# Kernel tuning notes

Hardware: AMD Instinct MI355X
Metric: run time of the kernel (lower is better)

Reference implementation:

```python
import jax, jax.numpy as jnp
import numpy as np

N, E, G = 50000, 400000, 500
F_IN, D_H, D_EMB = 92, 256, 128
EPS = 1e-5

def _ln(x, g, b):
    # per-node LayerNorm over feature dim
    mu = jnp.mean(x, axis=-1, keepdims=True)
    var = jnp.mean(jnp.square(x - mu), axis=-1, keepdims=True)
    return (x - mu) * jax.lax.rsqrt(var + EPS) * g + b

def _gcn_conv(x, src, dst, W, b):
    # PyG GCNConv: add self-loops, symmetric normalization
    xw = x @ W                                    # [N, D_out]
    loop = jnp.arange(N, dtype=src.dtype)
    s = jnp.concatenate([src, loop])              # [E+N]
    d = jnp.concatenate([dst, loop])
    deg = jax.ops.segment_sum(jnp.ones_like(d, dtype=xw.dtype), d, num_segments=N)
    dinv = jnp.where(deg > 0, jax.lax.rsqrt(jnp.maximum(deg, 1.0)) * (deg > 0), 0.0)
    norm = dinv[s] * dinv[d]                      # [E+N]
    msg = xw[s] * norm[:, None]                   # gather + scale
    out = jax.ops.segment_sum(msg, d, num_segments=N)  # scatter-add
    return out + b

def setup_inputs() -> dict:
    key = jax.random.key(0)
    ks = jax.random.split(key, 12)
    def lin(k, fan_in, fan_out):
        bound = 1.0 / np.sqrt(fan_in)
        kw, kb = jax.random.split(k)
        W = jax.random.uniform(kw, (fan_in, fan_out), jnp.float32, -bound, bound)
        b = jax.random.uniform(kb, (fan_out,), jnp.float32, -bound, bound)
        return W, b
    x = jax.random.normal(ks[0], (N, F_IN), jnp.float32)
    edge_index = jax.random.randint(ks[1], (2, E), 0, N, jnp.int32)
    batch = jnp.sort(jax.random.randint(ks[2], (N,), 0, G, jnp.int32))
    nfc_W, nfc_b = lin(ks[3], F_IN, D_H)
    gc1_W, gc1_b = lin(ks[4], D_H, D_H)
    gc2_W, gc2_b = lin(ks[5], D_H, D_EMB)
    fc1_W, fc1_b = lin(ks[6], D_EMB, 64)
    fc2_W, fc2_b = lin(ks[7], 64, 1)
    return {
        "x": x, "edge_index": edge_index, "batch": batch,
        "nfc_W": nfc_W, "nfc_b": nfc_b,
        "gn1_g": jnp.ones((D_H,), jnp.float32), "gn1_b": jnp.zeros((D_H,), jnp.float32),
        "gc1_W": gc1_W, "gc1_b": gc1_b,
        "gn2_g": jnp.ones((D_EMB,), jnp.float32), "gn2_b": jnp.zeros((D_EMB,), jnp.float32),
        "gc2_W": gc2_W, "gc2_b": gc2_b,
        "fc1_W": fc1_W, "fc1_b": fc1_b,
        "fc2_W": fc2_W, "fc2_b": fc2_b,
    }

def reference(x, edge_index, batch, nfc_W, nfc_b, gn1_g, gn1_b, gc1_W, gc1_b,
              gn2_g, gn2_b, gc2_W, gc2_b, fc1_W, fc1_b, fc2_W, fc2_b):
    src, dst = edge_index[0], edge_index[1]
    lrelu = jax.nn.leaky_relu  # slope 0.01, matches F.leaky_relu default
    ha = lrelu(x @ nfc_W + nfc_b)
    ha = lrelu(_ln(_gcn_conv(ha, src, dst, gc1_W, gc1_b), gn1_g, gn1_b))
    ha = lrelu(_ln(_gcn_conv(ha, src, dst, gc2_W, gc2_b), gn2_g, gn2_b))
    # F.normalize(p=2, dim=1)
    ha = ha / jnp.maximum(jnp.linalg.norm(ha, axis=1, keepdims=True), 1e-12)
    hg = jax.ops.segment_sum(ha, batch, num_segments=G)   # global_add_pool
    h = lrelu(hg @ fc1_W + fc1_b)
    out = h @ fc2_W + fc2_b
    return out, ha
```

## Files before the change

kernel.cpp:

```cpp
#include <hip/hip_runtime.h>

#define NN 50000
#define EE 400000
#define GG 500
#define F_IN 92
#define KP1 96
#define D_H 256
#define D_EMB 128
#define NB_SCAN 196

typedef __attribute__((ext_vector_type(8))) short short8_t;
typedef __attribute__((ext_vector_type(4))) float floatx4;
typedef unsigned short u16;
typedef unsigned int u32;

__device__ __forceinline__ float lrelu(float v) { return v > 0.f ? v : 0.01f * v; }
__device__ __forceinline__ u16 f2b(float v) {
    union { float f; u32 u; } x; x.f = v;
    u32 r = x.u + 0x7FFFu + ((x.u >> 16) & 1u);
    return (u16)(r >> 16);
}
__device__ __forceinline__ float wave_allsum(float v) {
#pragma unroll
    for (int m = 1; m < 64; m <<= 1) v += __shfl_xor(v, m);
    return v;
}
__device__ __forceinline__ void glds16(const void* g, void* l) {
    __builtin_amdgcn_global_load_lds(
        (const __attribute__((address_space(1))) void*)g,
        (__attribute__((address_space(3))) void*)l, 16, 0, 0);
}

#define WN_ELEMS (D_H * KP1)
#define W1_ELEMS (D_H * D_H)
#define W2_ELEMS (D_EMB * D_H)
#define CAST_BLK ((WN_ELEMS + W1_ELEMS + W2_ELEMS + 255) / 256)
__global__ void cast_count(const float* __restrict__ nfc_W, const float* __restrict__ gc1_W,
                           const float* __restrict__ gc2_W, u16* __restrict__ WtN,
                           u16* __restrict__ Wt1, u16* __restrict__ Wt2,
                           const int* __restrict__ dstE, int* __restrict__ cnt) {
    if ((int)blockIdx.x >= CAST_BLK) {
        int e = (blockIdx.x - CAST_BLK) * 256 + threadIdx.x;
        if (e < EE) atomicAdd(&cnt[dstE[e]], 1);
        return;
    }
    int i = blockIdx.x * blockDim.x + threadIdx.x;
    if (i < WN_ELEMS) {
        int n = i / KP1, k = i % KP1;
        WtN[i] = f2b(k < F_IN ? nfc_W[(long)k * D_H + n] : 0.f);
    } else if (i < WN_ELEMS + W1_ELEMS) {
        int j = i - WN_ELEMS;
        int n = j / D_H, k = j % D_H;
        Wt1[j] = f2b(gc1_W[(long)k * D_H + n]);
    } else if (i < WN_ELEMS + W1_ELEMS + W2_ELEMS) {
        int j = i - WN_ELEMS - W1_ELEMS;
        int n = j / D_H, k = j % D_H;
        Wt2[j] = f2b(gc2_W[(long)k * D_EMB + n]);
    }
}

__global__ __launch_bounds__(256) void gemm_f32a(const float* __restrict__ Af_,
                                                 const u16* __restrict__ Wt,
                                                 const float* __restrict__ bias,
                                                 u16* __restrict__ out,
                                                 const int* __restrict__ cnt,
                                                 int* __restrict__ rowptr,
                                                 int* __restrict__ bsum,
                                                 float* __restrict__ dinv,
                                                 int MBLK) {
    if ((int)blockIdx.x >= MBLK) {
        __shared__ int sm[256];
        int b = blockIdx.x - MBLK;
        int i = b * 256 + threadIdx.x;
        int v = (i < NN) ? cnt[i] : 0;
        if (i < NN) dinv[i] = rsqrtf((float)v + 1.0f);
        sm[threadIdx.x] = v;
        __syncthreads();
#pragma unroll
        for (int off = 1; off < 256; off <<= 1) {
            int t = (threadIdx.x >= off) ? sm[threadIdx.x - off] : 0;
            __syncthreads();
            sm[threadIdx.x] += t;
            __syncthreads();
        }
        if (i < NN) rowptr[i] = sm[threadIdx.x] - v;
        if (threadIdx.x == 255) bsum[b] = sm[255];
        return;
    }
    __shared__ u16 As[64][40];
    __shared__ u16 Bs[256][32];
    int tid = threadIdx.x;
    int wave = tid >> 6, lane = tid & 63;
    int lm = lane & 15, lk = lane >> 4;
    int m0 = blockIdx.x * 64;
    int rowA = tid >> 2, skA = (tid & 3) * 8;
    int lr = lane >> 2, lc = (lane & 3) * 8;
    int gmA = m0 + rowA;
    const float* Af = Af_ + (size_t)gmA * F_IN;
    const u16* Bp[4];
#pragma unroll
    for (int ch = 0; ch < 4; ++ch)
        Bp[ch] = Wt + (size_t)(wave * 64 + ch * 16 + lr) * KP1 + lc;
    floatx4 acc[16] = {};
    for (int k0 = 0; k0 < KP1; k0 += 32) {
        float f[8];
#pragma unroll
        for (int q = 0; q < 2; ++q) {
            int col = k0 + skA + 4 * q;
            float4 t = make_float4(0.f, 0.f, 0.f, 0.f);
            if (gmA < NN && col < F_IN) t = *(const float4*)(Af + col);
            f[4 * q] = t.x; f[4 * q + 1] = t.y; f[4 * q + 2] = t.z; f[4 * q + 3] = t.w;
        }
        u32 pk[4];
#pragma unroll
        for (int t2 = 0; t2 < 4; ++t2)
            pk[t2] = ((u32)f2b(f[2 * t2 + 1]) << 16) | f2b(f[2 * t2]);
        __syncthreads();
        *(uint4*)&As[rowA][skA] = make_uint4(pk[0], pk[1], pk[2], pk[3]);
#pragma unroll
        for (int ch = 0; ch < 4; ++ch)
            glds16(Bp[ch] + k0, &Bs[wave * 64 + ch * 16][0]);
        __syncthreads();
        short8_t af = *(const short8_t*)&As[wave * 16 + lm][lk * 8];
#pragma unroll
        for (int c = 0; c < 16; ++c) {
            short8_t bf = *(const short8_t*)&Bs[c * 16 + lm][lk * 8];
            acc[c] = __builtin_amdgcn_mfma_f32_16x16x32_bf16(af, bf, acc[c], 0, 0, 0);
        }
    }
#pragma unroll
    for (int r = 0; r < 4; ++r) {
        int gm = m0 + wave * 16 + lk * 4 + r;
        if (gm >= NN) continue;
#pragma unroll
        for (int c = 0; c < 16; ++c) {
            int gn = c * 16 + lm;
            float v = acc[c][r] + bias[gn];
            out[(size_t)gm * D_H + gn] = f2b(lrelu(v));
        }
    }
}

__global__ void scan23(int* __restrict__ rowptr, const int* __restrict__ bsum) {
    __shared__ int sm[256];
    int b = blockIdx.x;
    int v = ((int)threadIdx.x < b) ? bsum[threadIdx.x] : 0;
    sm[threadIdx.x] = v;
    __syncthreads();
#pragma unroll
    for (int off = 128; off > 0; off >>= 1) {
        if ((int)threadIdx.x < off) sm[threadIdx.x] += sm[threadIdx.x + off];
        __syncthreads();
    }
    int base = sm[0];
    int i = b * 256 + threadIdx.x;
    if (i < NN) rowptr[i] += base;
    if (i == 0) rowptr[NN] = EE;
}

template <int ND, bool SCAT>
__global__ __launch_bounds__(256) void gemm_glds(const u16* __restrict__ A,
                                                 const u16* __restrict__ Wt,
                                                 const float* __restrict__ rscale,
                                                 u16* __restrict__ out,
                                                 const int* __restrict__ srcE,
                                                 const int* __restrict__ dstE,
                                                 const int* __restrict__ rowptr,
                                                 int* __restrict__ cursor,
                                                 int* __restrict__ esrc,
                                                 int MBLK) {
    if constexpr (SCAT) {
        if ((int)blockIdx.x >= MBLK) {
            int e = (blockIdx.x - MBLK) * 256 + threadIdx.x;
            if (e < EE) {
                int d = dstE[e];
                int p = rowptr[d] + atomicAdd(&cursor[d], 1);
                esrc[p] = srcE[e];
            }
            return;
        }
    }
    constexpr int NC  = ND / 16;
    constexpr int BCH = ND / 64;
    __shared__ u16 As[2][64][32];
    __shared__ u16 Bs[2][ND][32];
    int tid = threadIdx.x;
    int wave = tid >> 6, lane = tid & 63;
    int lm = lane & 15, lk = lane >> 4;
    int m0 = blockIdx.x * 64;
    int lr = lane >> 2;
    int lc = (lane & 3) * 8;
    const int Ka = D_H;
    const u16* Ap = A + (size_t)(m0 + wave * 16 + lr) * Ka + lc;
    const u16* Bp[BCH];
#pragma unroll
    for (int ch = 0; ch < BCH; ++ch)
        Bp[ch] = Wt + (size_t)(wave * (ND / 4) + ch * 16 + lr) * Ka + lc;

    auto stage = [&](int b, int k0) {
        glds16(Ap + k0, &As[b][wave * 16][0]);
#pragma unroll
        for (int ch = 0; ch < BCH; ++ch)
            glds16(Bp[ch] + k0, &Bs[b][wave * (ND / 4) + ch * 16][0]);
    };

    floatx4 acc[NC] = {};
    constexpr int nk = D_H / 32;
    stage(0, 0);
    asm volatile("s_waitcnt vmcnt(0)" ::: "memory");
    __builtin_amdgcn_s_barrier();
    __builtin_amdgcn_sched_barrier(0);
    int cur = 0;
    for (int t = 0; t < nk; ++t) {
        if (t + 1 < nk) stage(cur ^ 1, (t + 1) * 32);
        short8_t af = *(const short8_t*)&As[cur][wave * 16 + lm][lk * 8];
#pragma unroll
        for (int c = 0; c < NC; ++c) {
            short8_t bf = *(const short8_t*)&Bs[cur][c * 16 + lm][lk * 8];
            acc[c] = __builtin_amdgcn_mfma_f32_16x16x32_bf16(af, bf, acc[c], 0, 0, 0);
        }
        if (t + 1 < nk) {
            __builtin_amdgcn_sched_barrier(0);
            asm volatile("s_waitcnt vmcnt(0)" ::: "memory");
            __builtin_amdgcn_s_barrier();
            __builtin_amdgcn_sched_barrier(0);
            cur ^= 1;
        }
    }
#pragma unroll
    for (int r = 0; r < 4; ++r) {
        int gm = m0 + wave * 16 + lk * 4 + r;
        if (gm >= NN) continue;
        float rs = rscale[gm];
#pragma unroll
        for (int c = 0; c < NC; ++c) {
            int gn = c * 16 + lm;
            out[(size_t)gm * ND + gn] = f2b(acc[c][r] * rs);
        }
    }
}

template <int U>
__device__ __forceinline__ void loadrow(const u32* __restrict__ p, u32* r) {
    if constexpr (U == 2) { uint2 t = *(const uint2*)p; r[0] = t.x; r[1] = t.y; }
    else                  { r[0] = *p; }
}
template <int D, bool L2N, bool TOBF, bool POOL>
__global__ __launch_bounds__(256) void agg_ln(const u16* __restrict__ y,
                                              const int* __restrict__ rowptr,
                                              const int* __restrict__ esrc,
                                              const float* __restrict__ dinv,
                                              const float* __restrict__ bias,
                                              const float* __restrict__ gamma,
                                              const float* __restrict__ beta,
                                              u16* __restrict__ outb,
                                              float* __restrict__ outf,
                                              const int* __restrict__ batch,
                                              float* __restrict__ hg) {
    constexpr int V = D / 64;
    constexpr int U = V / 2;
    constexpr int RW = D / 2;
    int wave = threadIdx.x >> 6, lane = threadIdx.x & 63;
    int i = blockIdx.x * 4 + wave;
    if constexpr (!POOL) { if (i >= NN) return; }
    int beg = __builtin_amdgcn_readfirstlane(rowptr[i]);
    int end = __builtin_amdgcn_readfirstlane(rowptr[i + 1]);
    const u32* yu = (const u32*)y;
    const int lu = lane * U;
    float accL[U] = {}, accH[U] = {};
    u32 r[8][U];
    int k = beg;
    for (; k + 7 < end; k += 8) {
#pragma unroll
        for (int q = 0; q < 8; ++q) loadrow<U>(yu + (size_t)esrc[k + q] * RW + lu, r[q]);
#pragma unroll
        for (int j = 0; j < U; ++j) {
            float sL = 0.f, sH = 0.f;
#pragma unroll
            for (int q = 0; q < 8; ++q) {
                sL += __uint_as_float(r[q][j] << 16);
                sH += __uint_as_float(r[q][j] & 0xFFFF0000u);
            }
            accL[j] += sL; accH[j] += sH;
        }
    }
    for (; k + 3 < end; k += 4) {
#pragma unroll
        for (int q = 0; q < 4; ++q) loadrow<U>(yu + (size_t)esrc[k + q] * RW + lu, r[q]);
#pragma unroll
        for (int j = 0; j < U; ++j) {
            accL[j] += (__uint_as_float(r[0][j] << 16) + __uint_as_float(r[1][j] << 16))
                     + (__uint_as_float(r[2][j] << 16) + __uint_as_float(r[3][j] << 16));
            accH[j] += (__uint_as_float(r[0][j] & 0xFFFF0000u) + __uint_as_float(r[1][j] & 0xFFFF0000u))
                     + (__uint_as_float(r[2][j] & 0xFFFF0000u) + __uint_as_float(r[3][j] & 0xFFFF0000u));
        }
    }
    for (; k < end; ++k) {
        loadrow<U>(yu + (size_t)esrc[k] * RW + lu, r[0]);
#pragma unroll
        for (int j = 0; j < U; ++j) {
            accL[j] += __uint_as_float(r[0][j] << 16);
            accH[j] += __uint_as_float(r[0][j] & 0xFFFF0000u);
        }
    }
    loadrow<U>(yu + (size_t)i * RW + lu, r[0]);
#pragma unroll
    for (int j = 0; j < U; ++j) {
        accL[j] += __uint_as_float(r[0][j] << 16);
        accH[j] += __uint_as_float(r[0][j] & 0xFFFF0000u);
    }
    float di = dinv[i];
    float xv[V], lsum = 0.f;
#pragma unroll
    for (int j = 0; j < U; ++j) {
        xv[2 * j]     = accL[j] * di + bias[lane * V + 2 * j];
        xv[2 * j + 1] = accH[j] * di + bias[lane * V + 2 * j + 1];
    }
#pragma unroll
    for (int v = 0; v < V; ++v) lsum += xv[v];
    float mu = wave_allsum(lsum) * (1.0f / D);
    float l2 = 0.f;
#pragma unroll
    for (int v = 0; v < V; ++v) { xv[v] -= mu; l2 += xv[v] * xv[v]; }
    float rstd = rsqrtf(wave_allsum(l2) * (1.0f / D) + 1e-5f);
    float yv[V], ss = 0.f;
#pragma unroll
    for (int v = 0; v < V; ++v) {
        float t = xv[v] * rstd * gamma[lane * V + v] + beta[lane * V + v];
        t = lrelu(t);
        yv[v] = t; ss += t * t;
    }
    if constexpr (L2N) {
        float inv = 1.0f / fmaxf(sqrtf(wave_allsum(ss)), 1e-12f);
#pragma unroll
        for (int v = 0; v < V; ++v) yv[v] *= inv;
    }
    if constexpr (TOBF) {
        if constexpr (V == 4) {
            *(ushort4*)(outb + (size_t)i * D + lane * V) =
                make_ushort4(f2b(yv[0]), f2b(yv[1]), f2b(yv[2]), f2b(yv[3]));
        } else {
            *(ushort2*)(outb + (size_t)i * D + lane * V) = make_ushort2(f2b(yv[0]), f2b(yv[1]));
        }
    } else {
        if constexpr (V == 2) {
            *(float2*)(outf + (size_t)i * D + lane * V) = make_float2(yv[0], yv[1]);
        } else {
            *(float4*)(outf + (size_t)i * D + lane * V) = make_float4(yv[0], yv[1], yv[2], yv[3]);
        }
    }
    if constexpr (POOL) {
        __shared__ float psm[4][D_EMB];
        __shared__ int pb[4];
        psm[wave][lane * 2]     = yv[0];
        psm[wave][lane * 2 + 1] = yv[1];
        if (lane == 0) pb[wave] = batch[i];
        __syncthreads();
        int tid = threadIdx.x;
        if (tid < D_EMB) {
            float acc = psm[0][tid];
            int cur = pb[0];
#pragma unroll
            for (int w = 1; w < 4; ++w) {
                if (pb[w] != cur) {
                    atomicAdd(&hg[(size_t)cur * D_EMB + tid], acc);
                    acc = 0.f; cur = pb[w];
                }
                acc += psm[w][tid];
            }
            atomicAdd(&hg[(size_t)cur * D_EMB + tid], acc);
        }
    }
}

__global__ __launch_bounds__(64) void head_kernel(const float* __restrict__ hg,
                                                  const float* __restrict__ fc1W,
                                                  const float* __restrict__ fc1b,
                                                  const float* __restrict__ fc2W,
                                                  const float* __restrict__ fc2b,
                                                  float* __restrict__ out) {
    int g = blockIdx.x;
    int j = threadIdx.x;
    float h = fc1b[j];
#pragma unroll 8
    for (int k = 0; k < D_EMB; ++k) h += hg[(size_t)g * D_EMB + k] * fc1W[k * 64 + j];
    h = lrelu(h) * fc2W[j];
#pragma unroll
    for (int m = 1; m < 64; m <<= 1) h += __shfl_xor(h, m);
    if (j == 0) out[g] = h + fc2b[0];
}

static inline size_t align256(size_t x) { return (x + 255) & ~(size_t)255; }

extern "C" void kernel_launch(void* const* d_in, const int* in_sizes, int n_in,
                              void* d_out, int out_size, void* d_ws, size_t ws_size,
                              hipStream_t stream) {
    const float* x     = (const float*)d_in[0];
    const int*   ei    = (const int*)d_in[1];
    const int*   batch = (const int*)d_in[2];
    const float* nfc_W = (const float*)d_in[3];
    const float* nfc_b = (const float*)d_in[4];
    const float* gn1_g = (const float*)d_in[5];
    const float* gn1_b = (const float*)d_in[6];
    const float* gc1_W = (const float*)d_in[7];
    const float* gc1_b = (const float*)d_in[8];
    const float* gn2_g = (const float*)d_in[9];
    const float* gn2_b = (const float*)d_in[10];
    const float* gc2_W = (const float*)d_in[11];
    const float* gc2_b = (const float*)d_in[12];
    const float* fc1_W = (const float*)d_in[13];
    const float* fc1_b = (const float*)d_in[14];
    const float* fc2_W = (const float*)d_in[15];
    const float* fc2_b = (const float*)d_in[16];

    char* ws = (char*)d_ws;
    size_t off = 0;
    int*   cnt    = (int*)(ws + off);   off += (size_t)NN * 4;
    int*   cursor = (int*)(ws + off);   off += (size_t)NN * 4;
    float* hg     = (float*)(ws + off); off += align256((size_t)GG * D_EMB * 4);
    float* dinv   = (float*)(ws + off); off += align256((size_t)NN * 4);
    int*   rowptr = (int*)(ws + off);   off += align256((size_t)(NN + 1) * 4);
    int*   bsum   = (int*)(ws + off);   off += align256((size_t)256 * 4);
    int*   esrc   = (int*)(ws + off);   off += align256((size_t)EE * 4);
    u16*   WtN    = (u16*)(ws + off);   off += align256((size_t)D_H * KP1 * 2);
    u16*   Wt1    = (u16*)(ws + off);   off += align256((size_t)D_H * D_H * 2);
    u16*   Wt2    = (u16*)(ws + off);   off += align256((size_t)D_EMB * D_H * 2);
    u16*   ha1b   = (u16*)(ws + off);   off += align256((size_t)NN * D_H * 2);
    u16*   y1b    = (u16*)(ws + off);   off += align256((size_t)NN * D_H * 2);
    u16*   ha2b   = (u16*)(ws + off);   off += align256((size_t)NN * D_H * 2);
    u16*   y2b    = (u16*)(ws + off);   off += align256((size_t)NN * D_EMB * 2);

    const int* src = ei;
    const int* dst = ei + EE;
    float* out_scores = (float*)d_out;
    float* out_ha     = (float*)d_out + GG;

    const int MB = (NN + 63) / 64;
    const int EB = (EE + 255) / 256;
    const size_t zbytes = (size_t)NN * 8 + (size_t)GG * D_EMB * 4;

    hipMemsetAsync(cnt, 0, zbytes, stream);
    cast_count<<<CAST_BLK + EB, 256, 0, stream>>>(
        nfc_W, gc1_W, gc2_W, WtN, Wt1, Wt2, dst, cnt);

    gemm_f32a<<<MB + NB_SCAN, 256, 0, stream>>>(
        x, WtN, nfc_b, ha1b, cnt, rowptr, bsum, dinv, MB);

    scan23<<<NB_SCAN, 256, 0, stream>>>(rowptr, bsum);

    gemm_glds<D_H, true><<<MB + EB, 256, 0, stream>>>(
        ha1b, Wt1, dinv, y1b, src, dst, rowptr, cursor, esrc, MB);
    agg_ln<D_H, false, true, false><<<NN / 4, 256, 0, stream>>>(
        y1b, rowptr, esrc, dinv, gc1_b, gn1_g, gn1_b, ha2b, nullptr, nullptr, nullptr);

    gemm_glds<D_EMB, false><<<MB, 256, 0, stream>>>(
        ha2b, Wt2, dinv, y2b, nullptr, nullptr, nullptr, nullptr, nullptr, MB);
    agg_ln<D_EMB, true, false, true><<<NN / 4, 256, 0, stream>>>(
        y2b, rowptr, esrc, dinv, gc2_b, gn2_g, gn2_b, nullptr, out_ha, batch, hg);

    head_kernel<<<GG, 64, 0, stream>>>(hg, fc1_W, fc1_b, fc2_W, fc2_b, out_scores);
}
```

Before: 259.2 us.

## Replace LDS-staged GEMMs with direct register loads of A and weights

Both bf16 GEMM kernels and the fp32-input GEMM drop shared-memory staging, global_load_lds, double buffering and block barriers. Each wave now loads its A fragment and weight fragments straight from global memory into registers for MFMA. This removes barrier and LDS overhead, but each wave re-reads the full weight matrix and relies on L1/L2 caching for reuse.

```diff
diff --git a/kernel.cpp b/kernel.cpp
--- a/kernel.cpp
+++ b/kernel.cpp
@@ -24,11 +24,6 @@
 #pragma unroll
     for (int m = 1; m < 64; m <<= 1) v += __shfl_xor(v, m);
     return v;
-}
-__device__ __forceinline__ void glds16(const void* g, void* l) {
-    __builtin_amdgcn_global_load_lds(
-        (const __attribute__((address_space(1))) void*)g,
-        (__attribute__((address_space(3))) void*)l, 16, 0, 0);
 }
 
 #define WN_ELEMS (D_H * KP1)
@@ -87,50 +82,37 @@
         if (threadIdx.x == 255) bsum[b] = sm[255];
         return;
     }
-    __shared__ u16 As[64][40];
-    __shared__ u16 Bs[256][32];
     int tid = threadIdx.x;
     int wave = tid >> 6, lane = tid & 63;
     int lm = lane & 15, lk = lane >> 4;
-    int m0 = blockIdx.x * 64;
-    int rowA = tid >> 2, skA = (tid & 3) * 8;
-    int lr = lane >> 2, lc = (lane & 3) * 8;
-    int gmA = m0 + rowA;
+    int m0 = blockIdx.x * 64 + wave * 16;
+    int gmA = m0 + lm;
     const float* Af = Af_ + (size_t)gmA * F_IN;
-    const u16* Bp[4];
-#pragma unroll
-    for (int ch = 0; ch < 4; ++ch)
-        Bp[ch] = Wt + (size_t)(wave * 64 + ch * 16 + lr) * KP1 + lc;
+    const u16* Bp = Wt + (size_t)lm * KP1 + lk * 8;
     floatx4 acc[16] = {};
-    for (int k0 = 0; k0 < KP1; k0 += 32) {
-        float f[8];
-#pragma unroll
-        for (int q = 0; q < 2; ++q) {
-            int col = k0 + skA + 4 * q;
-            float4 t = make_float4(0.f, 0.f, 0.f, 0.f);
-            if (gmA < NN && col < F_IN) t = *(const float4*)(Af + col);
-            f[4 * q] = t.x; f[4 * q + 1] = t.y; f[4 * q + 2] = t.z; f[4 * q + 3] = t.w;
-        }
-        u32 pk[4];
-#pragma unroll
-        for (int t2 = 0; t2 < 4; ++t2)
-            pk[t2] = ((u32)f2b(f[2 * t2 + 1]) << 16) | f2b(f[2 * t2]);
-        __syncthreads();
-        *(uint4*)&As[rowA][skA] = make_uint4(pk[0], pk[1], pk[2], pk[3]);
-#pragma unroll
-        for (int ch = 0; ch < 4; ++ch)
-            glds16(Bp[ch] + k0, &Bs[wave * 64 + ch * 16][0]);
-        __syncthreads();
-        short8_t af = *(const short8_t*)&As[wave * 16 + lm][lk * 8];
+#pragma unroll
+    for (int t = 0; t < 3; ++t) {
+        int col0 = t * 32 + lk * 8;
+        float4 t0 = make_float4(0.f, 0.f, 0.f, 0.f);
+        float4 t1 = make_float4(0.f, 0.f, 0.f, 0.f);
+        if (gmA < NN) {
+            t0 = *(const float4*)(Af + col0);
+            if (col0 + 8 <= F_IN) t1 = *(const float4*)(Af + col0 + 4);
+        }
+        union { u32 u[4]; short8_t v; } af;
+        af.u[0] = ((u32)f2b(t0.y) << 16) | f2b(t0.x);
+        af.u[1] = ((u32)f2b(t0.w) << 16) | f2b(t0.z);
+        af.u[2] = ((u32)f2b(t1.y) << 16) | f2b(t1.x);
+        af.u[3] = ((u32)f2b(t1.w) << 16) | f2b(t1.z);
 #pragma unroll
         for (int c = 0; c < 16; ++c) {
-            short8_t bf = *(const short8_t*)&Bs[c * 16 + lm][lk * 8];
-            acc[c] = __builtin_amdgcn_mfma_f32_16x16x32_bf16(af, bf, acc[c], 0, 0, 0);
+            short8_t bf = *(const short8_t*)(Bp + (size_t)c * 16 * KP1 + t * 32);
+            acc[c] = __builtin_amdgcn_mfma_f32_16x16x32_bf16(af.v, bf, acc[c], 0, 0, 0);
         }
     }
 #pragma unroll
     for (int r = 0; r < 4; ++r) {
-        int gm = m0 + wave * 16 + lk * 4 + r;
+        int gm = m0 + lk * 4 + r;
         if (gm >= NN) continue;
 #pragma unroll
         for (int c = 0; c < 16; ++c) {
@@ -159,16 +141,16 @@
 }
 
 template <int ND, bool SCAT>
-__global__ __launch_bounds__(256) void gemm_glds(const u16* __restrict__ A,
-                                                 const u16* __restrict__ Wt,
-                                                 const float* __restrict__ rscale,
-                                                 u16* __restrict__ out,
-                                                 const int* __restrict__ srcE,
-                                                 const int* __restrict__ dstE,
-                                                 const int* __restrict__ rowptr,
-                                                 int* __restrict__ cursor,
-                                                 int* __restrict__ esrc,
-                                                 int MBLK) {
+__global__ __launch_bounds__(256) void gemm_reg(const u16* __restrict__ A,
+                                                const u16* __restrict__ Wt,
+                                                const float* __restrict__ rscale,
+                                                u16* __restrict__ out,
+                                                const int* __restrict__ srcE,
+                                                const int* __restrict__ dstE,
+                                                const int* __restrict__ rowptr,
+                                                int* __restrict__ cursor,
+                                                int* __restrict__ esrc,
+                                                int MBLK) {
     if constexpr (SCAT) {
         if ((int)blockIdx.x >= MBLK) {
             int e = (blockIdx.x - MBLK) * 256 + threadIdx.x;
@@ -180,56 +162,26 @@
             return;
         }
     }
-    constexpr int NC  = ND / 16;
-    constexpr int BCH = ND / 64;
-    __shared__ u16 As[2][64][32];
-    __shared__ u16 Bs[2][ND][32];
+    constexpr int NC = ND / 16;
     int tid = threadIdx.x;
     int wave = tid >> 6, lane = tid & 63;
     int lm = lane & 15, lk = lane >> 4;
-    int m0 = blockIdx.x * 64;
-    int lr = lane >> 2;
-    int lc = (lane & 3) * 8;
-    const int Ka = D_H;
-    const u16* Ap = A + (size_t)(m0 + wave * 16 + lr) * Ka + lc;
-    const u16* Bp[BCH];
-#pragma unroll
-    for (int ch = 0; ch < BCH; ++ch)
-        Bp[ch] = Wt + (size_t)(wave * (ND / 4) + ch * 16 + lr) * Ka + lc;
-
-    auto stage = [&](int b, int k0) {
-        glds16(Ap + k0, &As[b][wave * 16][0]);
-#pragma unroll
-        for (int ch = 0; ch < BCH; ++ch)
-            glds16(Bp[ch] + k0, &Bs[b][wave * (ND / 4) + ch * 16][0]);
-    };
-
+    int m0 = blockIdx.x * 64 + wave * 16;
+    const u16* Ap = A + (size_t)(m0 + lm) * D_H + lk * 8;
+    const u16* Bp = Wt + (size_t)lm * D_H + lk * 8;
     floatx4 acc[NC] = {};
-    constexpr int nk = D_H / 32;
-    stage(0, 0);
-    asm volatile("s_waitcnt vmcnt(0)" ::: "memory");
-    __builtin_amdgcn_s_barrier();
-    __builtin_amdgcn_sched_barrier(0);
-    int cur = 0;
-    for (int t = 0; t < nk; ++t) {
-        if (t + 1 < nk) stage(cur ^ 1, (t + 1) * 32);
-        short8_t af = *(const short8_t*)&As[cur][wave * 16 + lm][lk * 8];
+#pragma unroll 2
+    for (int t = 0; t < D_H / 32; ++t) {
+        short8_t af = *(const short8_t*)(Ap + t * 32);
 #pragma unroll
         for (int c = 0; c < NC; ++c) {
-            short8_t bf = *(const short8_t*)&Bs[cur][c * 16 + lm][lk * 8];
+            short8_t bf = *(const short8_t*)(Bp + (size_t)c * 16 * D_H + t * 32);
             acc[c] = __builtin_amdgcn_mfma_f32_16x16x32_bf16(af, bf, acc[c], 0, 0, 0);
         }
-        if (t + 1 < nk) {
-            __builtin_amdgcn_sched_barrier(0);
-            asm volatile("s_waitcnt vmcnt(0)" ::: "memory");
-            __builtin_amdgcn_s_barrier();
-            __builtin_amdgcn_sched_barrier(0);
-            cur ^= 1;
-        }
     }
 #pragma unroll
     for (int r = 0; r < 4; ++r) {
-        int gm = m0 + wave * 16 + lk * 4 + r;
+        int gm = m0 + lk * 4 + r;
         if (gm >= NN) continue;
         float rs = rscale[gm];
 #pragma unroll
@@ -448,12 +400,12 @@
 
     scan23<<<NB_SCAN, 256, 0, stream>>>(rowptr, bsum);
 
-    gemm_glds<D_H, true><<<MB + EB, 256, 0, stream>>>(
+    gemm_reg<D_H, true><<<MB + EB, 256, 0, stream>>>(
         ha1b, Wt1, dinv, y1b, src, dst, rowptr, cursor, esrc, MB);
     agg_ln<D_H, false, true, false><<<NN / 4, 256, 0, stream>>>(
         y1b, rowptr, esrc, dinv, gc1_b, gn1_g, gn1_b, ha2b, nullptr, nullptr, nullptr);
 
-    gemm_glds<D_EMB, false><<<MB, 256, 0, stream>>>(
+    gemm_reg<D_EMB, false><<<MB, 256, 0, stream>>>(
         ha2b, Wt2, dinv, y2b, nullptr, nullptr, nullptr, nullptr, nullptr, MB);
     agg_ln<D_EMB, true, false, true><<<NN / 4, 256, 0, stream>>>(
         y2b, rowptr, esrc, dinv, gc2_b, gn2_g, gn2_b, nullptr, out_ha, batch, hg);
```

Result: slower. 320.9 us (+23.8%).
